# Performance work log

Hardware: AMD Instinct MI355X
Metric: run time of the kernel (lower is better)

The kernel has to match this reference:

```python
import jax, jax.numpy as jnp
import numpy as np

B, T, E = 64, 64, 256
S, ENC = 128, 1024
RNN, ATT, DENSE = 1024, 1024, 8000


def setup_inputs() -> dict:
    key = jax.random.key(0)
    ks = jax.random.split(key, 16)
    s = 0.02
    return {
        "initial_input": jax.random.normal(ks[0], (B, T, E), jnp.float32),
        "hidden": jax.random.normal(ks[1], (B, RNN), jnp.float32),
        "cell": jax.random.normal(ks[2], (B, RNN), jnp.float32),
        "encoder_output": jax.random.normal(ks[3], (B, S, ENC), jnp.float32),
        "W1": jax.random.normal(ks[4], (RNN, ATT), jnp.float32) * s,
        "b1": jnp.zeros((ATT,), jnp.float32),
        "W2": jax.random.normal(ks[5], (ENC, ATT), jnp.float32) * s,
        "b2": jnp.zeros((ATT,), jnp.float32),
        "V": jax.random.normal(ks[6], (ATT, 1), jnp.float32) * s,
        "bV": jnp.zeros((1,), jnp.float32),
        "kernel": jax.random.normal(ks[7], (ENC + E, 4 * RNN), jnp.float32) * s,
        "rkernel": jax.random.normal(ks[8], (RNN, 4 * RNN), jnp.float32) * s,
        "bias": jnp.zeros((4 * RNN,), jnp.float32),
        "Wd": jax.random.normal(ks[9], (RNN, DENSE), jnp.float32) * s,
        "bd": jnp.zeros((DENSE,), jnp.float32),
        "seq_len": T,
    }


def _decode(initial_input, hidden, cell, encoder_output,
            W1, b1, W2, b2, V, bV, kernel, rkernel, bias, Wd, bd):
    # Keys W2(encoder_output) are step-independent: precompute once. [B,S,ATT]
    keys = jnp.einsum('bse,ea->bsa', encoder_output, W2) + b2

    def step(carry, x_t):
        h, c = carry
        # Bahdanau attention: score = V^T tanh(W1 h + W2 enc)
        q = h @ W1 + b1                                  # [B,ATT]
        score = jnp.tanh(q[:, None, :] + keys) @ V + bV   # [B,S,1]
        attn = jax.nn.softmax(score, axis=1)              # [B,S,1]
        ctx = jnp.sum(attn * encoder_output, axis=1)      # [B,ENC]
        # LSTM cell (Keras gate order i,f,g,o; sigmoid/tanh activations)
        inp = jnp.concatenate([ctx, x_t], axis=-1)        # [B,ENC+E]
        z = inp @ kernel + h @ rkernel + bias              # [B,4*RNN]
        i, f, g, o = jnp.split(z, 4, axis=-1)
        i = jax.nn.sigmoid(i)
        f = jax.nn.sigmoid(f)
        g = jnp.tanh(g)
        o = jax.nn.sigmoid(o)
        c_new = f * c + i * g
        h_new = o * jnp.tanh(c_new)
        logits = h_new @ Wd + bd                           # [B,DENSE]
        return (h_new, c_new), logits

    xs = jnp.swapaxes(initial_input, 0, 1)  # [T,B,E]
    (h, c), logits = jax.lax.scan(step, (hidden, cell), xs)
    outputs = jnp.swapaxes(logits, 0, 1)    # [B,T,DENSE]
    return outputs, h, c


def reference(initial_input, hidden, cell, encoder_output,
              W1, b1, W2, b2, V, bV, kernel, rkernel, bias, Wd, bd, seq_len):
    # seq_len == initial_input.shape[1] (static); the Python loop in the
    # original is expressed as an efficient lax.scan over decode steps.
    return _decode(initial_input[:, :seq_len, :], hidden, cell, encoder_output,
                   W1, b1, W2, b2, V, bV, kernel, rkernel, bias, Wd, bd)
```

## Files before the change

kernel.cpp:

```cpp
#include <hip/hip_runtime.h>
#include <hip/hip_bf16.h>
#include <stdint.h>


typedef __attribute__((ext_vector_type(8))) short short8;
typedef __attribute__((ext_vector_type(4))) float floatx4;
typedef __attribute__((ext_vector_type(4))) unsigned short ushortx4;

__device__ __forceinline__ float b2f(unsigned short u) {
    union { unsigned int i; float f; } v; v.i = ((unsigned int)u) << 16; return v.f;
}
__device__ __forceinline__ unsigned short f2b(float f) {
    union { float f; unsigned int i; } v; v.f = f;
    unsigned int r = v.i + 0x7fffu + ((v.i >> 16) & 1u);
    return (unsigned short)(r >> 16);
}
__device__ __forceinline__ float ftanh(float x) {
    x = fminf(15.f, fmaxf(-15.f, x));
    float e = __expf(2.f * x);
    return (e - 1.f) * __builtin_amdgcn_rcpf(e + 1.f);
}
__device__ __forceinline__ float fsig(float x) {
    return __builtin_amdgcn_rcpf(1.f + __expf(-x));
}
__device__ __forceinline__ void ld_lds16(const void* g, void* l) {
    __builtin_amdgcn_global_load_lds((const __attribute__((address_space(1))) void*)g,
                                     (__attribute__((address_space(3))) void*)l, 16, 0, 0);
}

__global__ __launch_bounds__(256) void conv_f32_bf16(
    const float* __restrict__ src, unsigned short* __restrict__ dst, int n4)
{
    int i = blockIdx.x * 256 + threadIdx.x;
    if (i < n4) {
        float4 v = ((const float4*)src)[i];
        ushortx4 o;
        o[0] = f2b(v.x); o[1] = f2b(v.y); o[2] = f2b(v.z); o[3] = f2b(v.w);
        ((ushortx4*)dst)[i] = o;
    }
}

__global__ __launch_bounds__(256) void transpose_conv(
    const float* __restrict__ src, int srcld,
    unsigned short* __restrict__ dst, int dstld, int coloff, int perm)
{
    __shared__ float tile[32][33];
    const int k0 = blockIdx.y * 32, n0 = blockIdx.x * 32;
    const int r = threadIdx.x >> 3, c = (threadIdx.x & 7) * 4;
    int n = n0 + c;
    int cn = perm ? ((((n >> 4) & 3) << 10) | ((n >> 6) << 4) | (n & 15)) : n;
    float4 v = *(const float4*)&src[(size_t)(k0 + r) * srcld + cn];
    tile[r][c + 0] = v.x; tile[r][c + 1] = v.y;
    tile[r][c + 2] = v.z; tile[r][c + 3] = v.w;
    __syncthreads();
    const int nr = threadIdx.x >> 3, kc = (threadIdx.x & 7) * 4;
    ushortx4 o;
    o[0] = f2b(tile[kc + 0][nr]);
    o[1] = f2b(tile[kc + 1][nr]);
    o[2] = f2b(tile[kc + 2][nr]);
    o[3] = f2b(tile[kc + 3][nr]);
    *(ushortx4*)&dst[(size_t)(n0 + nr) * dstld + coloff + k0 + kc] = o;
}

__global__ __launch_bounds__(256) void gemm_bf16_128(
    const unsigned short* __restrict__ A, int lda,
    const unsigned short* __restrict__ BT, int ldbt, int K,
    float* __restrict__ Cf, unsigned short* __restrict__ Cb,
    int ldc, int ncols, const float* __restrict__ bias)
{
    __shared__ __align__(16) unsigned short As[128 * 32];
    __shared__ __align__(16) unsigned short Bs[128 * 32];
    const int tid = threadIdx.x, wave = tid >> 6, lane = tid & 63;
    const int q = lane >> 4, lm = lane & 15;
    const int wr = wave >> 1, wc = wave & 1;
    const int m0 = blockIdx.y * 128, n0 = blockIdx.x * 128;
    const int srow = lane >> 2;
    const int gch = (lane & 3) ^ ((lane >> 3) & 3);
    const unsigned short* Ag0 = A + (size_t)(m0 + wave * 32 + srow) * lda + gch * 8;
    const unsigned short* Ag1 = Ag0 + (size_t)16 * lda;
    const unsigned short* Bg0 = BT + (size_t)(n0 + wave * 32 + srow) * ldbt + gch * 8;
    const unsigned short* Bg1 = Bg0 + (size_t)16 * ldbt;
    unsigned short* Al0 = &As[(wave * 32) * 32];
    unsigned short* Al1 = &As[(wave * 32 + 16) * 32];
    unsigned short* Bl0 = &Bs[(wave * 32) * 32];
    unsigned short* Bl1 = &Bs[(wave * 32 + 16) * 32];

    const floatx4 z4 = {0.f, 0.f, 0.f, 0.f};
    floatx4 acc[4][4];
#pragma unroll
    for (int i = 0; i < 4; i++)
#pragma unroll
        for (int j = 0; j < 4; j++) acc[i][j] = z4;
    const int ach = ((q ^ ((lm >> 1) & 3))) * 8;

    for (int kb = 0; kb < K; kb += 32) {
        ld_lds16(Ag0 + kb, Al0);
        ld_lds16(Ag1 + kb, Al1);
        ld_lds16(Bg0 + kb, Bl0);
        ld_lds16(Bg1 + kb, Bl1);
        __syncthreads();
        short8 a[4], b[4];
#pragma unroll
        for (int i = 0; i < 4; i++) a[i] = *(const short8*)&As[(wr * 64 + i * 16 + lm) * 32 + ach];
#pragma unroll
        for (int j = 0; j < 4; j++) b[j] = *(const short8*)&Bs[(wc * 64 + j * 16 + lm) * 32 + ach];
#pragma unroll
        for (int i = 0; i < 4; i++)
#pragma unroll
            for (int j = 0; j < 4; j++)
                acc[i][j] = __builtin_amdgcn_mfma_f32_16x16x32_bf16(a[i], b[j], acc[i][j], 0, 0, 0);
        __syncthreads();
    }
    const int rb = m0 + wr * 64 + q * 4;
#pragma unroll
    for (int i = 0; i < 4; i++) {
#pragma unroll
        for (int j = 0; j < 4; j++) {
            int col = n0 + wc * 64 + j * 16 + lm;
            if (col < ncols) {
                float bv = bias ? bias[col] : 0.f;
#pragma unroll
                for (int r = 0; r < 4; r++) {
                    float v = acc[i][j][r] + bv;
                    size_t idx = (size_t)(rb + i * 16 + r) * ldc + col;
                    if (Cf) Cf[idx] = v;
                    if (Cb) Cb[idx] = f2b(v);
                }
            }
        }
    }
}

__global__ __launch_bounds__(256) void gemm64_split(
    const unsigned short* __restrict__ A, int lda,
    const unsigned short* __restrict__ BT, int ldbt,
    int kchunk, float* __restrict__ Cpart, int ldc)
{
    __shared__ __align__(16) unsigned short As[2][64 * 32];
    __shared__ __align__(16) unsigned short Bs[2][64 * 32];
    const int tid = threadIdx.x, wave = tid >> 6, lane = tid & 63;
    const int q = lane >> 4, lm = lane & 15;
    const int n0 = blockIdx.x * 64;
    const int k0 = blockIdx.z * kchunk;
    const int srow = lane >> 2;
    const int gch = (lane & 3) ^ ((lane >> 3) & 3);
    const unsigned short* Ag = A + (size_t)(wave * 16 + srow) * lda + k0 + gch * 8;
    const unsigned short* Bg = BT + (size_t)(n0 + wave * 16 + srow) * ldbt + k0 + gch * 8;
    const int loff = (wave * 16) * 32;
    const floatx4 z4 = {0.f, 0.f, 0.f, 0.f};
    floatx4 acc0 = z4, acc1 = z4, acc2 = z4, acc3 = z4;
    const int ach = ((q ^ ((lm >> 1) & 3))) * 8;
    const int nit = kchunk >> 5;

    ld_lds16(Ag, &As[0][loff]);
    ld_lds16(Bg, &Bs[0][loff]);
    __syncthreads();
    for (int it = 0; it < nit; ++it) {
        const int cur = it & 1;
        if (it + 1 < nit) {
            ld_lds16(Ag + (it + 1) * 32, &As[cur ^ 1][loff]);
            ld_lds16(Bg + (it + 1) * 32, &Bs[cur ^ 1][loff]);
        }
        short8 a  = *(const short8*)&As[cur][(wave * 16 + lm) * 32 + ach];
        short8 b0 = *(const short8*)&Bs[cur][(0 * 16 + lm) * 32 + ach];
        short8 b1 = *(const short8*)&Bs[cur][(1 * 16 + lm) * 32 + ach];
        short8 b2 = *(const short8*)&Bs[cur][(2 * 16 + lm) * 32 + ach];
        short8 b3 = *(const short8*)&Bs[cur][(3 * 16 + lm) * 32 + ach];
        acc0 = __builtin_amdgcn_mfma_f32_16x16x32_bf16(a, b0, acc0, 0, 0, 0);
        acc1 = __builtin_amdgcn_mfma_f32_16x16x32_bf16(a, b1, acc1, 0, 0, 0);
        acc2 = __builtin_amdgcn_mfma_f32_16x16x32_bf16(a, b2, acc2, 0, 0, 0);
        acc3 = __builtin_amdgcn_mfma_f32_16x16x32_bf16(a, b3, acc3, 0, 0, 0);
        __syncthreads();
    }
    float* Cp = Cpart + (size_t)blockIdx.z * 64 * ldc;
    const int rb = wave * 16 + q * 4;
    floatx4 accs[4] = {acc0, acc1, acc2, acc3};
#pragma unroll
    for (int i = 0; i < 4; i++) {
        int col = n0 + i * 16 + lm;
#pragma unroll
        for (int r = 0; r < 4; r++) Cp[(size_t)(rb + r) * ldc + col] = accs[i][r];
    }
}

__global__ __launch_bounds__(256) void init_hc(
    const float* __restrict__ hidden, const float* __restrict__ cell,
    float* __restrict__ hf, float* __restrict__ cb, unsigned short* __restrict__ hbf)
{
    int idx = blockIdx.x * 256 + threadIdx.x;
    float h = hidden[idx], c = cell[idx];
    hf[idx] = h; cb[idx] = c; hbf[idx] = f2b(h);
}

__global__ __launch_bounds__(256) void attn_scores(
    const float* __restrict__ qzh, const float* __restrict__ b1,
    const unsigned short* __restrict__ keys,
    const float* __restrict__ V, const float* __restrict__ bV,
    float* __restrict__ sc)
{
    __shared__ float qs[1024];
    __shared__ float vs[1024];
    const int b = blockIdx.y, sg = blockIdx.x;
    const int tid = threadIdx.x, wave = tid >> 6, lane = tid & 63;
    {
        float4 a0 = ((const float4*)(qzh + (size_t)b * 5120))[tid];
        float4 a1 = ((const float4*)(qzh + 327680 + (size_t)b * 5120))[tid];
        float4 ab = ((const float4*)b1)[tid];
        float4 av = ((const float4*)V)[tid];
        float4 r;
        r.x = a0.x + a1.x + ab.x; r.y = a0.y + a1.y + ab.y;
        r.z = a0.z + a1.z + ab.z; r.w = a0.w + a1.w + ab.w;
        *(float4*)&qs[tid * 4] = r;
        *(float4*)&vs[tid * 4] = av;
    }
    __syncthreads();
    float qr[16], vr[16];
#pragma unroll
    for (int i = 0; i < 4; i++) {
        float4 tq = *(const float4*)&qs[lane * 16 + i * 4];
        float4 tv = *(const float4*)&vs[lane * 16 + i * 4];
        qr[i * 4 + 0] = tq.x; qr[i * 4 + 1] = tq.y; qr[i * 4 + 2] = tq.z; qr[i * 4 + 3] = tq.w;
        vr[i * 4 + 0] = tv.x; vr[i * 4 + 1] = tv.y; vr[i * 4 + 2] = tv.z; vr[i * 4 + 3] = tv.w;
    }
    const float bv0 = bV[0];
#pragma unroll
    for (int i = 0; i < 4; i++) {
        const int s = sg * 16 + wave * 4 + i;
        const uint4* kp = (const uint4*)(keys + ((size_t)(b * 128 + s)) * 1024 + lane * 16);
        uint4 k0 = kp[0], k1 = kp[1];
        float kf[16];
        kf[0] = b2f((unsigned short)(k0.x & 0xffff)); kf[1] = b2f((unsigned short)(k0.x >> 16));
        kf[2] = b2f((unsigned short)(k0.y & 0xffff)); kf[3] = b2f((unsigned short)(k0.y >> 16));
        kf[4] = b2f((unsigned short)(k0.z & 0xffff)); kf[5] = b2f((unsigned short)(k0.z >> 16));
        kf[6] = b2f((unsigned short)(k0.w & 0xffff)); kf[7] = b2f((unsigned short)(k0.w >> 16));
        kf[8] = b2f((unsigned short)(k1.x & 0xffff)); kf[9] = b2f((unsigned short)(k1.x >> 16));
        kf[10] = b2f((unsigned short)(k1.y & 0xffff)); kf[11] = b2f((unsigned short)(k1.y >> 16));
        kf[12] = b2f((unsigned short)(k1.z & 0xffff)); kf[13] = b2f((unsigned short)(k1.z >> 16));
        kf[14] = b2f((unsigned short)(k1.w & 0xffff)); kf[15] = b2f((unsigned short)(k1.w >> 16));
        float part = 0.f;
#pragma unroll
        for (int j = 0; j < 16; j++) part += vr[j] * ftanh(qr[j] + kf[j]);
#pragma unroll
        for (int off = 32; off; off >>= 1) part += __shfl_xor(part, off);
        if (lane == 0) sc[b * 128 + s] = part + bv0;
    }
}

__global__ __launch_bounds__(256) void softmax_ctx(
    const float* __restrict__ sc, const unsigned short* __restrict__ enc_bf,
    const float* __restrict__ x, unsigned short* __restrict__ Axc, int t)
{
    __shared__ float attnv[128];
    __shared__ float red[4][64][2];
    __shared__ float smax_s, ssum_s;
    const int b = blockIdx.y, chunk = blockIdx.x;
    const int tid = threadIdx.x, wave = tid >> 6, lane = tid & 63;
    float sv = 0.f;
    if (tid < 128) { sv = sc[b * 128 + tid]; attnv[tid] = sv; }
    __syncthreads();
    if (tid < 64) {
        float m = fmaxf(attnv[tid], attnv[tid + 64]);
#pragma unroll
        for (int off = 32; off; off >>= 1) m = fmaxf(m, __shfl_xor(m, off));
        if (tid == 0) smax_s = m;
    }
    __syncthreads();
    if (tid < 128) attnv[tid] = __expf(sv - smax_s);
    __syncthreads();
    if (tid < 64) {
        float s2 = attnv[tid] + attnv[tid + 64];
#pragma unroll
        for (int off = 32; off; off >>= 1) s2 += __shfl_xor(s2, off);
        if (tid == 0) ssum_s = s2;
    }
    if (chunk < 2 && tid < 64) {
        int c2 = chunk * 128 + tid * 2;
        float x0 = x[((size_t)b * 64 + t) * 256 + c2];
        float x1 = x[((size_t)b * 64 + t) * 256 + c2 + 1];
        *(unsigned int*)&Axc[b * 1280 + 1024 + c2] =
            (unsigned int)f2b(x0) | ((unsigned int)f2b(x1) << 16);
    }
    const unsigned int* ep = (const unsigned int*)enc_bf + (size_t)b * 65536 + chunk * 64 + lane;
    __syncthreads();
    float ax = 0.f, ay = 0.f;
#pragma unroll 8
    for (int i = 0; i < 32; i++) {
        int s = wave * 32 + i;
        float a = attnv[s];
        unsigned int u = ep[(size_t)s * 512];
        ax += a * b2f((unsigned short)(u & 0xffff));
        ay += a * b2f((unsigned short)(u >> 16));
    }
    red[wave][lane][0] = ax; red[wave][lane][1] = ay;
    __syncthreads();
    if (tid < 64) {
        float rs = __builtin_amdgcn_rcpf(ssum_s);
        float fx = (red[0][lane][0] + red[1][lane][0] + red[2][lane][0] + red[3][lane][0]) * rs;
        float fy = (red[0][lane][1] + red[1][lane][1] + red[2][lane][1] + red[3][lane][1]) * rs;
        *(unsigned int*)&Axc[b * 1280 + chunk * 128 + lane * 2] =
            (unsigned int)f2b(fx) | ((unsigned int)f2b(fy) << 16);
    }
}

__global__ __launch_bounds__(512) void gemm_gates(
    const unsigned short* __restrict__ Axc,
    const unsigned short* __restrict__ KcT,
    const float* __restrict__ qzh, const float* __restrict__ bz,
    float* __restrict__ cb, float* __restrict__ hf,
    unsigned short* __restrict__ hbf, unsigned short* __restrict__ Hall, int t)
{
    __shared__ __align__(16) unsigned short As[2][2][64 * 32];
    __shared__ __align__(16) unsigned short Bs[2][2][64 * 32];
    __shared__ float red[4 * 64 * 16];
    const int tid = threadIdx.x, wave = tid >> 6, lane = tid & 63;
    const int q = lane >> 4, lm = lane & 15;
    const int h = wave >> 2, wm = wave & 3;
    const int bx = blockIdx.x;
    const int srow = lane >> 2;
    const int gch = (lane & 3) ^ ((lane >> 3) & 3);
    const unsigned short* Ag = Axc + (size_t)(wm * 16 + srow) * 1280 + h * 640 + gch * 8;
    const unsigned short* Bg = KcT + (size_t)(bx * 64 + wm * 16 + srow) * 1280 + h * 640 + gch * 8;
    const int loff = (wm * 16) * 32;
    const floatx4 z4 = {0.f, 0.f, 0.f, 0.f};
    floatx4 acc0 = z4, acc1 = z4, acc2 = z4, acc3 = z4;
    const int ach = ((q ^ ((lm >> 1) & 3))) * 8;

    ld_lds16(Ag, &As[0][h][loff]);
    ld_lds16(Bg, &Bs[0][h][loff]);
    __syncthreads();
#pragma unroll 1
    for (int it = 0; it < 20; ++it) {
        const int cur = it & 1;
        if (it < 19) {
            ld_lds16(Ag + (it + 1) * 32, &As[cur ^ 1][h][loff]);
            ld_lds16(Bg + (it + 1) * 32, &Bs[cur ^ 1][h][loff]);
        }
        short8 a  = *(const short8*)&As[cur][h][(wm * 16 + lm) * 32 + ach];
        short8 b0 = *(const short8*)&Bs[cur][h][(0 * 16 + lm) * 32 + ach];
        short8 b1 = *(const short8*)&Bs[cur][h][(1 * 16 + lm) * 32 + ach];
        short8 b2 = *(const short8*)&Bs[cur][h][(2 * 16 + lm) * 32 + ach];
        short8 b3 = *(const short8*)&Bs[cur][h][(3 * 16 + lm) * 32 + ach];
        acc0 = __builtin_amdgcn_mfma_f32_16x16x32_bf16(a, b0, acc0, 0, 0, 0);
        acc1 = __builtin_amdgcn_mfma_f32_16x16x32_bf16(a, b1, acc1, 0, 0, 0);
        acc2 = __builtin_amdgcn_mfma_f32_16x16x32_bf16(a, b2, acc2, 0, 0, 0);
        acc3 = __builtin_amdgcn_mfma_f32_16x16x32_bf16(a, b3, acc3, 0, 0, 0);
        __syncthreads();
    }
    if (h == 1) {
        float* rp = &red[(wm * 64 + lane) * 16];
        *(floatx4*)&rp[0]  = acc0; *(floatx4*)&rp[4]  = acc1;
        *(floatx4*)&rp[8]  = acc2; *(floatx4*)&rp[12] = acc3;
    }
    __syncthreads();
    if (h == 0) {
        const float* rp = &red[(wm * 64 + lane) * 16];
        acc0 += *(const floatx4*)&rp[0];
        acc1 += *(const floatx4*)&rp[4];
        acc2 += *(const floatx4*)&rp[8];
        acc3 += *(const floatx4*)&rp[12];
        const int col = bx * 16 + lm;
        const float bzi = bz[col], bzf = bz[1024 + col];
        const float bzg = bz[2048 + col], bzo = bz[3072 + col];
#pragma unroll
        for (int r = 0; r < 4; ++r) {
            const int b = wm * 16 + q * 4 + r;
            const float* z0 = qzh + (size_t)b * 5120 + 1024;
            const float* z1 = qzh + 327680 + (size_t)b * 5120 + 1024;
            float zi = acc0[r] + z0[col] + z1[col] + bzi;
            float zf = acc1[r] + z0[1024 + col] + z1[1024 + col] + bzf;
            float zg = acc2[r] + z0[2048 + col] + z1[2048 + col] + bzg;
            float zo = acc3[r] + z0[3072 + col] + z1[3072 + col] + bzo;
            float ii = fsig(zi), ff = fsig(zf), gg = ftanh(zg), oo = fsig(zo);
            const int idx = b * 1024 + col;
            float cn = ff * cb[idx] + ii * gg;
            float hn = oo * ftanh(cn);
            cb[idx] = cn; hf[idx] = hn;
            unsigned short hb = f2b(hn);
            hbf[idx] = hb;
            Hall[((size_t)b * 64 + t) * 1024 + col] = hb;
        }
    }
}

__global__ __launch_bounds__(256) void tail_k(
    const float* __restrict__ hf, const float* __restrict__ cb, float* __restrict__ out)
{
    int i = blockIdx.x * 256 + threadIdx.x;
    if (i < 65536) out[32768000 + i] = hf[i];
    else out[32768000 + i] = cb[i - 65536];
}

extern "C" void kernel_launch(void* const* d_in, const int* in_sizes, int n_in,
                              void* d_out, int out_size, void* d_ws, size_t ws_size,
                              hipStream_t stream)
{
    const float* x      = (const float*)d_in[0];
    const float* hidden = (const float*)d_in[1];
    const float* cell   = (const float*)d_in[2];
    const float* enc    = (const float*)d_in[3];
    const float* W1     = (const float*)d_in[4];
    const float* b1     = (const float*)d_in[5];
    const float* W2     = (const float*)d_in[6];
    const float* b2     = (const float*)d_in[7];
    const float* V      = (const float*)d_in[8];
    const float* bV     = (const float*)d_in[9];
    const float* Wk     = (const float*)d_in[10];
    const float* rk     = (const float*)d_in[11];
    const float* bz     = (const float*)d_in[12];
    const float* Wd     = (const float*)d_in[13];
    const float* bd     = (const float*)d_in[14];
    float* out = (float*)d_out;

    char* ws = (char*)d_ws;
    unsigned short* enc_bf  = (unsigned short*)(ws + 0);
    unsigned short* keys_bf = (unsigned short*)(ws + 16777216);
    unsigned short* WcT     = (unsigned short*)(ws + 33554432);
    unsigned short* KcT     = (unsigned short*)(ws + 44040192);
    unsigned short* WdT     = (unsigned short*)(ws + 54525952);
    unsigned short* Hall    = (unsigned short*)(ws + 71041024);
    unsigned short* W2T     = Hall;
    unsigned short* hbf     = (unsigned short*)(ws + 79429632);
    unsigned short* Axc     = (unsigned short*)(ws + 79560704);
    float* qzh   = (float*)(ws + 79724544);
    float* scbuf = (float*)(ws + 84443136);
    float* hf    = (float*)(ws + 84475904);
    float* cb    = (float*)(ws + 84738048);

    conv_f32_bf16<<<8192, 256, 0, stream>>>(enc, enc_bf, 8388608 / 4);
    transpose_conv<<<dim3(32, 32),  256, 0, stream>>>(W2, 1024, W2T, 1024, 0, 0);
    transpose_conv<<<dim3(32, 32),  256, 0, stream>>>(W1, 1024, WcT, 1024, 0, 0);
    transpose_conv<<<dim3(128, 32), 256, 0, stream>>>(rk, 4096, WcT + 1024 * 1024, 1024, 0, 0);
    transpose_conv<<<dim3(128, 32), 256, 0, stream>>>(Wk, 4096, KcT, 1280, 0, 1);
    transpose_conv<<<dim3(128, 8),  256, 0, stream>>>(Wk + 1024 * 4096, 4096, KcT, 1280, 1024, 1);
    transpose_conv<<<dim3(250, 32), 256, 0, stream>>>(Wd, 8000, WdT, 1024, 0, 0);
    init_hc<<<256, 256, 0, stream>>>(hidden, cell, hf, cb, hbf);

    gemm_bf16_128<<<dim3(8, 64), 256, 0, stream>>>(enc_bf, 1024, W2T, 1024, 1024,
                                                   nullptr, keys_bf, 1024, 1024, b2);

    for (int t = 0; t < 64; t++) {
        gemm64_split<<<dim3(80, 1, 2), 256, 0, stream>>>(hbf, 1024, WcT, 1024, 512, qzh, 5120);
        attn_scores<<<dim3(8, 64), 256, 0, stream>>>(qzh, b1, keys_bf, V, bV, scbuf);
        softmax_ctx<<<dim3(8, 64), 256, 0, stream>>>(scbuf, enc_bf, x, Axc, t);
        gemm_gates<<<64, 512, 0, stream>>>(Axc, KcT, qzh, bz, cb, hf, hbf, Hall, t);
    }

    gemm_bf16_128<<<dim3(63, 32), 256, 0, stream>>>(Hall, 1024, WdT, 1024, 1024,
                                                    out, nullptr, 8000, 8000, bd);
    tail_k<<<512, 256, 0, stream>>>(hf, cb, out);
}
```

Baseline: 2.696 ms.

## Fold recurrent h@rkernel into gates GEMM and deepen LDS pipelines

The recurrent h@rkernel product moves out of the per-step split GEMM and into the gates GEMM. The transposed recurrent kernel is concatenated with the input kernel along K (2304), and softmax_ctx copies the bf16 hidden state into the activation row. The q GEMM now computes only h@W1, with a 4-way K split over 16 column tiles instead of a 2-way split over 80, and attn_scores sums four partials. Both GEMMs switch from a double-buffered LDS loop with a full barrier per iteration to a 4-stage ring with 3 loads in flight, using explicit vmcnt waits plus barriers. This cuts per-step fp32 partial traffic and launch work, but the gates kernel's K loop grows from 20 to 36 iterations on only 64 blocks, which lengthens the serial critical path.

```diff
diff --git a/kernel.cpp b/kernel.cpp
--- a/kernel.cpp
+++ b/kernel.cpp
@@ -136,8 +136,8 @@
     const unsigned short* __restrict__ BT, int ldbt,
     int kchunk, float* __restrict__ Cpart, int ldc)
 {
-    __shared__ __align__(16) unsigned short As[2][64 * 32];
-    __shared__ __align__(16) unsigned short Bs[2][64 * 32];
+    __shared__ __align__(16) unsigned short As[4][64 * 32];
+    __shared__ __align__(16) unsigned short Bs[4][64 * 32];
     const int tid = threadIdx.x, wave = tid >> 6, lane = tid & 63;
     const int q = lane >> 4, lm = lane & 15;
     const int n0 = blockIdx.x * 64;
@@ -152,25 +152,32 @@
     const int ach = ((q ^ ((lm >> 1) & 3))) * 8;
     const int nit = kchunk >> 5;
 
-    ld_lds16(Ag, &As[0][loff]);
-    ld_lds16(Bg, &Bs[0][loff]);
-    __syncthreads();
+#pragma unroll
+    for (int p = 0; p < 3; ++p) {
+        if (p < nit) {
+            ld_lds16(Ag + p * 32, &As[p][loff]);
+            ld_lds16(Bg + p * 32, &Bs[p][loff]);
+        }
+    }
     for (int it = 0; it < nit; ++it) {
-        const int cur = it & 1;
-        if (it + 1 < nit) {
-            ld_lds16(Ag + (it + 1) * 32, &As[cur ^ 1][loff]);
-            ld_lds16(Bg + (it + 1) * 32, &Bs[cur ^ 1][loff]);
+        const int st = it & 3;
+        if (it + 2 < nit)      asm volatile("s_waitcnt vmcnt(4)\n\ts_barrier" ::: "memory");
+        else if (it + 1 < nit) asm volatile("s_waitcnt vmcnt(2)\n\ts_barrier" ::: "memory");
+        else                   asm volatile("s_waitcnt vmcnt(0)\n\ts_barrier" ::: "memory");
+        if (it + 3 < nit) {
+            const int sn = (it + 3) & 3;
+            ld_lds16(Ag + (it + 3) * 32, &As[sn][loff]);
+            ld_lds16(Bg + (it + 3) * 32, &Bs[sn][loff]);
         }
-        short8 a  = *(const short8*)&As[cur][(wave * 16 + lm) * 32 + ach];
-        short8 b0 = *(const short8*)&Bs[cur][(0 * 16 + lm) * 32 + ach];
-        short8 b1 = *(const short8*)&Bs[cur][(1 * 16 + lm) * 32 + ach];
-        short8 b2 = *(const short8*)&Bs[cur][(2 * 16 + lm) * 32 + ach];
-        short8 b3 = *(const short8*)&Bs[cur][(3 * 16 + lm) * 32 + ach];
+        short8 a  = *(const short8*)&As[st][(wave * 16 + lm) * 32 + ach];
+        short8 b0 = *(const short8*)&Bs[st][(0 * 16 + lm) * 32 + ach];
+        short8 b1 = *(const short8*)&Bs[st][(1 * 16 + lm) * 32 + ach];
+        short8 b2 = *(const short8*)&Bs[st][(2 * 16 + lm) * 32 + ach];
+        short8 b3 = *(const short8*)&Bs[st][(3 * 16 + lm) * 32 + ach];
         acc0 = __builtin_amdgcn_mfma_f32_16x16x32_bf16(a, b0, acc0, 0, 0, 0);
         acc1 = __builtin_amdgcn_mfma_f32_16x16x32_bf16(a, b1, acc1, 0, 0, 0);
         acc2 = __builtin_amdgcn_mfma_f32_16x16x32_bf16(a, b2, acc2, 0, 0, 0);
         acc3 = __builtin_amdgcn_mfma_f32_16x16x32_bf16(a, b3, acc3, 0, 0, 0);
-        __syncthreads();
     }
     float* Cp = Cpart + (size_t)blockIdx.z * 64 * ldc;
     const int rb = wave * 16 + q * 4;
@@ -193,7 +200,7 @@
 }
 
 __global__ __launch_bounds__(256) void attn_scores(
-    const float* __restrict__ qzh, const float* __restrict__ b1,
+    const float* __restrict__ qp, const float* __restrict__ b1,
     const unsigned short* __restrict__ keys,
     const float* __restrict__ V, const float* __restrict__ bV,
     float* __restrict__ sc)
@@ -203,13 +210,17 @@
     const int b = blockIdx.y, sg = blockIdx.x;
     const int tid = threadIdx.x, wave = tid >> 6, lane = tid & 63;
     {
-        float4 a0 = ((const float4*)(qzh + (size_t)b * 5120))[tid];
-        float4 a1 = ((const float4*)(qzh + 327680 + (size_t)b * 5120))[tid];
+        float4 a0 = ((const float4*)(qp + (size_t)b * 1024))[tid];
+        float4 a1 = ((const float4*)(qp + 65536 + (size_t)b * 1024))[tid];
+        float4 a2 = ((const float4*)(qp + 131072 + (size_t)b * 1024))[tid];
+        float4 a3 = ((const float4*)(qp + 196608 + (size_t)b * 1024))[tid];
         float4 ab = ((const float4*)b1)[tid];
         float4 av = ((const float4*)V)[tid];
         float4 r;
-        r.x = a0.x + a1.x + ab.x; r.y = a0.y + a1.y + ab.y;
-        r.z = a0.z + a1.z + ab.z; r.w = a0.w + a1.w + ab.w;
+        r.x = a0.x + a1.x + a2.x + a3.x + ab.x;
+        r.y = a0.y + a1.y + a2.y + a3.y + ab.y;
+        r.z = a0.z + a1.z + a2.z + a3.z + ab.z;
+        r.w = a0.w + a1.w + a2.w + a3.w + ab.w;
         *(float4*)&qs[tid * 4] = r;
         *(float4*)&vs[tid * 4] = av;
     }
@@ -248,7 +259,8 @@
 
 __global__ __launch_bounds__(256) void softmax_ctx(
     const float* __restrict__ sc, const unsigned short* __restrict__ enc_bf,
-    const float* __restrict__ x, unsigned short* __restrict__ Axc, int t)
+    const float* __restrict__ x, const unsigned short* __restrict__ hbf,
+    unsigned short* __restrict__ Axc, int t)
 {
     __shared__ float attnv[128];
     __shared__ float red[4][64][2];
@@ -277,8 +289,13 @@
         int c2 = chunk * 128 + tid * 2;
         float x0 = x[((size_t)b * 64 + t) * 256 + c2];
         float x1 = x[((size_t)b * 64 + t) * 256 + c2 + 1];
-        *(unsigned int*)&Axc[b * 1280 + 1024 + c2] =
+        *(unsigned int*)&Axc[b * 2304 + 1024 + c2] =
             (unsigned int)f2b(x0) | ((unsigned int)f2b(x1) << 16);
+    }
+    if (tid < 64) {
+        int c2 = chunk * 128 + tid * 2;
+        *(unsigned int*)&Axc[b * 2304 + 1280 + c2] =
+            *(const unsigned int*)&hbf[b * 1024 + c2];
     }
     const unsigned int* ep = (const unsigned int*)enc_bf + (size_t)b * 65536 + chunk * 64 + lane;
     __syncthreads();
@@ -297,55 +314,64 @@
         float rs = __builtin_amdgcn_rcpf(ssum_s);
         float fx = (red[0][lane][0] + red[1][lane][0] + red[2][lane][0] + red[3][lane][0]) * rs;
         float fy = (red[0][lane][1] + red[1][lane][1] + red[2][lane][1] + red[3][lane][1]) * rs;
-        *(unsigned int*)&Axc[b * 1280 + chunk * 128 + lane * 2] =
+        *(unsigned int*)&Axc[b * 2304 + chunk * 128 + lane * 2] =
             (unsigned int)f2b(fx) | ((unsigned int)f2b(fy) << 16);
     }
 }
 
 __global__ __launch_bounds__(512) void gemm_gates(
     const unsigned short* __restrict__ Axc,
-    const unsigned short* __restrict__ KcT,
-    const float* __restrict__ qzh, const float* __restrict__ bz,
+    const unsigned short* __restrict__ KRT,
+    const float* __restrict__ bz,
     float* __restrict__ cb, float* __restrict__ hf,
     unsigned short* __restrict__ hbf, unsigned short* __restrict__ Hall, int t)
 {
-    __shared__ __align__(16) unsigned short As[2][2][64 * 32];
-    __shared__ __align__(16) unsigned short Bs[2][2][64 * 32];
-    __shared__ float red[4 * 64 * 16];
+    __shared__ __align__(16) char smem[65536];
+    unsigned short* As = (unsigned short*)smem;
+    unsigned short* Bs = (unsigned short*)(smem + 32768);
+    float* red = (float*)smem;
     const int tid = threadIdx.x, wave = tid >> 6, lane = tid & 63;
     const int q = lane >> 4, lm = lane & 15;
     const int h = wave >> 2, wm = wave & 3;
     const int bx = blockIdx.x;
     const int srow = lane >> 2;
     const int gch = (lane & 3) ^ ((lane >> 3) & 3);
-    const unsigned short* Ag = Axc + (size_t)(wm * 16 + srow) * 1280 + h * 640 + gch * 8;
-    const unsigned short* Bg = KcT + (size_t)(bx * 64 + wm * 16 + srow) * 1280 + h * 640 + gch * 8;
-    const int loff = (wm * 16) * 32;
+    const unsigned short* Ag = Axc + (size_t)(wm * 16 + srow) * 2304 + h * 1152 + gch * 8;
+    const unsigned short* Bg = KRT + (size_t)(bx * 64 + wm * 16 + srow) * 2304 + h * 1152 + gch * 8;
+    const int tileoff = h * 2048;
+    const int ldoff = tileoff + (wm * 16) * 32;
     const floatx4 z4 = {0.f, 0.f, 0.f, 0.f};
     floatx4 acc0 = z4, acc1 = z4, acc2 = z4, acc3 = z4;
     const int ach = ((q ^ ((lm >> 1) & 3))) * 8;
 
-    ld_lds16(Ag, &As[0][h][loff]);
-    ld_lds16(Bg, &Bs[0][h][loff]);
-    __syncthreads();
-#pragma unroll 1
-    for (int it = 0; it < 20; ++it) {
-        const int cur = it & 1;
-        if (it < 19) {
-            ld_lds16(Ag + (it + 1) * 32, &As[cur ^ 1][h][loff]);
-            ld_lds16(Bg + (it + 1) * 32, &Bs[cur ^ 1][h][loff]);
+#pragma unroll
+    for (int p = 0; p < 3; ++p) {
+        ld_lds16(Ag + p * 32, &As[p * 4096 + ldoff]);
+        ld_lds16(Bg + p * 32, &Bs[p * 4096 + ldoff]);
+    }
+    for (int it = 0; it < 36; ++it) {
+        const int st = it & 3;
+        if (it < 34)       asm volatile("s_waitcnt vmcnt(4)\n\ts_barrier" ::: "memory");
+        else if (it == 34) asm volatile("s_waitcnt vmcnt(2)\n\ts_barrier" ::: "memory");
+        else               asm volatile("s_waitcnt vmcnt(0)\n\ts_barrier" ::: "memory");
+        if (it + 3 < 36) {
+            const int sn = (it + 3) & 3;
+            ld_lds16(Ag + (it + 3) * 32, &As[sn * 4096 + ldoff]);
+            ld_lds16(Bg + (it + 3) * 32, &Bs[sn * 4096 + ldoff]);
         }
-        short8 a  = *(const short8*)&As[cur][h][(wm * 16 + lm) * 32 + ach];
-        short8 b0 = *(const short8*)&Bs[cur][h][(0 * 16 + lm) * 32 + ach];
-        short8 b1 = *(const short8*)&Bs[cur][h][(1 * 16 + lm) * 32 + ach];
-        short8 b2 = *(const short8*)&Bs[cur][h][(2 * 16 + lm) * 32 + ach];
-        short8 b3 = *(const short8*)&Bs[cur][h][(3 * 16 + lm) * 32 + ach];
+        const unsigned short* Ast = &As[st * 4096 + tileoff];
+        const unsigned short* Bst = &Bs[st * 4096 + tileoff];
+        short8 a  = *(const short8*)&Ast[(wm * 16 + lm) * 32 + ach];
+        short8 b0 = *(const short8*)&Bst[(0 * 16 + lm) * 32 + ach];
+        short8 b1 = *(const short8*)&Bst[(1 * 16 + lm) * 32 + ach];
+        short8 b2 = *(const short8*)&Bst[(2 * 16 + lm) * 32 + ach];
+        short8 b3 = *(const short8*)&Bst[(3 * 16 + lm) * 32 + ach];
         acc0 = __builtin_amdgcn_mfma_f32_16x16x32_bf16(a, b0, acc0, 0, 0, 0);
         acc1 = __builtin_amdgcn_mfma_f32_16x16x32_bf16(a, b1, acc1, 0, 0, 0);
         acc2 = __builtin_amdgcn_mfma_f32_16x16x32_bf16(a, b2, acc2, 0, 0, 0);
         acc3 = __builtin_amdgcn_mfma_f32_16x16x32_bf16(a, b3, acc3, 0, 0, 0);
-        __syncthreads();
-    }
+    }
+    __syncthreads();
     if (h == 1) {
         float* rp = &red[(wm * 64 + lane) * 16];
         *(floatx4*)&rp[0]  = acc0; *(floatx4*)&rp[4]  = acc1;
@@ -364,12 +390,10 @@
 #pragma unroll
         for (int r = 0; r < 4; ++r) {
             const int b = wm * 16 + q * 4 + r;
-            const float* z0 = qzh + (size_t)b * 5120 + 1024;
-            const float* z1 = qzh + 327680 + (size_t)b * 5120 + 1024;
-            float zi = acc0[r] + z0[col] + z1[col] + bzi;
-            float zf = acc1[r] + z0[1024 + col] + z1[1024 + col] + bzf;
-            float zg = acc2[r] + z0[2048 + col] + z1[2048 + col] + bzg;
-            float zo = acc3[r] + z0[3072 + col] + z1[3072 + col] + bzo;
+            float zi = acc0[r] + bzi;
+            float zf = acc1[r] + bzf;
+            float zg = acc2[r] + bzg;
+            float zo = acc3[r] + bzo;
             float ii = fsig(zi), ff = fsig(zf), gg = ftanh(zg), oo = fsig(zo);
             const int idx = b * 1024 + col;
             float cn = ff * cb[idx] + ii * gg;
@@ -414,24 +438,24 @@
     char* ws = (char*)d_ws;
     unsigned short* enc_bf  = (unsigned short*)(ws + 0);
     unsigned short* keys_bf = (unsigned short*)(ws + 16777216);
-    unsigned short* WcT     = (unsigned short*)(ws + 33554432);
-    unsigned short* KcT     = (unsigned short*)(ws + 44040192);
+    unsigned short* W1T     = (unsigned short*)(ws + 33554432);
+    unsigned short* KRT     = (unsigned short*)(ws + 35651584);
     unsigned short* WdT     = (unsigned short*)(ws + 54525952);
     unsigned short* Hall    = (unsigned short*)(ws + 71041024);
     unsigned short* W2T     = Hall;
-    unsigned short* hbf     = (unsigned short*)(ws + 79429632);
-    unsigned short* Axc     = (unsigned short*)(ws + 79560704);
-    float* qzh   = (float*)(ws + 79724544);
-    float* scbuf = (float*)(ws + 84443136);
-    float* hf    = (float*)(ws + 84475904);
-    float* cb    = (float*)(ws + 84738048);
+    unsigned short* Axc     = (unsigned short*)(ws + 79429632);
+    float* qp    = (float*)(ws + 79724544);
+    float* scbuf = (float*)(ws + 80773120);
+    unsigned short* hbf     = (unsigned short*)(ws + 80805888);
+    float* hf    = (float*)(ws + 80936960);
+    float* cb    = (float*)(ws + 81199104);
 
     conv_f32_bf16<<<8192, 256, 0, stream>>>(enc, enc_bf, 8388608 / 4);
     transpose_conv<<<dim3(32, 32),  256, 0, stream>>>(W2, 1024, W2T, 1024, 0, 0);
-    transpose_conv<<<dim3(32, 32),  256, 0, stream>>>(W1, 1024, WcT, 1024, 0, 0);
-    transpose_conv<<<dim3(128, 32), 256, 0, stream>>>(rk, 4096, WcT + 1024 * 1024, 1024, 0, 0);
-    transpose_conv<<<dim3(128, 32), 256, 0, stream>>>(Wk, 4096, KcT, 1280, 0, 1);
-    transpose_conv<<<dim3(128, 8),  256, 0, stream>>>(Wk + 1024 * 4096, 4096, KcT, 1280, 1024, 1);
+    transpose_conv<<<dim3(32, 32),  256, 0, stream>>>(W1, 1024, W1T, 1024, 0, 0);
+    transpose_conv<<<dim3(128, 32), 256, 0, stream>>>(Wk, 4096, KRT, 2304, 0, 1);
+    transpose_conv<<<dim3(128, 8),  256, 0, stream>>>(Wk + 1024 * 4096, 4096, KRT, 2304, 1024, 1);
+    transpose_conv<<<dim3(128, 32), 256, 0, stream>>>(rk, 4096, KRT, 2304, 1280, 1);
     transpose_conv<<<dim3(250, 32), 256, 0, stream>>>(Wd, 8000, WdT, 1024, 0, 0);
     init_hc<<<256, 256, 0, stream>>>(hidden, cell, hf, cb, hbf);
 
@@ -439,10 +463,10 @@
                                                    nullptr, keys_bf, 1024, 1024, b2);
 
     for (int t = 0; t < 64; t++) {
-        gemm64_split<<<dim3(80, 1, 2), 256, 0, stream>>>(hbf, 1024, WcT, 1024, 512, qzh, 5120);
-        attn_scores<<<dim3(8, 64), 256, 0, stream>>>(qzh, b1, keys_bf, V, bV, scbuf);
-        softmax_ctx<<<dim3(8, 64), 256, 0, stream>>>(scbuf, enc_bf, x, Axc, t);
-        gemm_gates<<<64, 512, 0, stream>>>(Axc, KcT, qzh, bz, cb, hf, hbf, Hall, t);
+        gemm64_split<<<dim3(16, 1, 4), 256, 0, stream>>>(hbf, 1024, W1T, 1024, 256, qp, 1024);
+        attn_scores<<<dim3(8, 64), 256, 0, stream>>>(qp, b1, keys_bf, V, bV, scbuf);
+        softmax_ctx<<<dim3(8, 64), 256, 0, stream>>>(scbuf, enc_bf, x, hbf, Axc, t);
+        gemm_gates<<<64, 512, 0, stream>>>(Axc, KRT, bz, cb, hf, hbf, Hall, t);
     }
 
     gemm_bf16_128<<<dim3(63, 32), 256, 0, stream>>>(Hall, 1024, WdT, 1024, 1024,
```

New measurement: 2.372 ms. 12.0% less time.
